# Kernel optimization log

Measured on AMD Instinct MI355X. Metric: run time of the kernel, lower is better.

The kernel has to match this reference:

```python
import jax, jax.numpy as jnp
import numpy as np

B, T, N, F, C, H, O = 4, 8, 4096, 32, 32, 64, 1
RADIUS = 50.0   # adjacency_threshold on pairwise distance
EPS = 1e-5      # batchnorm eps


def setup_inputs() -> dict:
    key = jax.random.key(0)
    ks = jax.random.split(key, 8)
    x = jax.random.normal(ks[0], (B, T, N, F), jnp.float32)
    # dist_mat from random 2D node locations in a 1000x1000 area; avg degree ~32
    loc = jax.random.uniform(ks[1], (N, 2), jnp.float32) * 1000.0
    d2 = jnp.sum((loc[:, None, :] - loc[None, :, :]) ** 2, axis=-1)  # [N,N]
    adj = (d2 < RADIUS ** 2).astype(jnp.float32)                     # includes self (d=0)
    dinv = 1.0 / jnp.sqrt(jnp.maximum(adj.sum(-1), 1.0))
    adj_norm = adj * dinv[:, None] * dinv[None, :]                   # D^-1/2 A D^-1/2
    s = 0.05
    return dict(
        x=x,
        adj_norm=adj_norm,
        bn_gamma=jnp.ones((F,), jnp.float32),
        bn_beta=jnp.zeros((F,), jnp.float32),
        W_gcn=jax.random.normal(ks[2], (F, C), jnp.float32) * s,
        b_gcn=jnp.zeros((C,), jnp.float32),
        W_ih=jax.random.normal(ks[3], (C, 3 * H), jnp.float32) * s,
        W_hh=jax.random.normal(ks[4], (H, 3 * H), jnp.float32) * s,
        b_ih=jnp.zeros((3 * H,), jnp.float32),
        b_hh=jnp.zeros((3 * H,), jnp.float32),
        W_dense=jax.random.normal(ks[5], (H, O), jnp.float32) * s,
        b_dense=jnp.zeros((O,), jnp.float32),
    )


def reference(x, adj_norm, bn_gamma, bn_beta, W_gcn, b_gcn, W_ih, W_hh, b_ih, b_hh, W_dense, b_dense):
    # BatchNorm2d over feature channel (training-mode batch stats, biased var)
    mean = x.mean(axis=(0, 1, 2))
    var = x.var(axis=(0, 1, 2))
    xn = (x - mean) * jax.lax.rsqrt(var + EPS) * bn_gamma + bn_beta  # [B,T,N,F]
    # GCN association (same math every timestep -> batch over T)
    ya = jnp.einsum('mn,btnf->btmf', adj_norm, xn)                   # neighbor aggregate
    y = jnp.einsum('btnf,fc->btnc', ya, W_gcn) + b_gcn               # [B,T,N,C]
    # precompute input-gate projections, then scan GRU cell over time
    gi = jnp.einsum('btnc,ch->btnh', y, W_ih) + b_ih                 # [B,T,N,3H]
    gi = jnp.transpose(gi, (1, 0, 2, 3))                             # [T,B,N,3H]

    def step(h, g):
        gh = h @ W_hh + b_hh
        r = jax.nn.sigmoid(g[..., :H] + gh[..., :H])
        z = jax.nn.sigmoid(g[..., H:2 * H] + gh[..., H:2 * H])
        n = jnp.tanh(g[..., 2 * H:] + r * gh[..., 2 * H:])
        h_new = (1.0 - z) * n + z * h
        return h_new, h_new

    h0 = jnp.zeros((B, N, H), x.dtype)
    _, hs = jax.lax.scan(step, h0, gi)                               # [T,B,N,H]
    out = jnp.transpose(hs, (1, 0, 2, 3)) @ W_dense + b_dense        # [B,T,N,O]
    return out
```

## Files before the change

kernel.cpp:

```cpp
#include <hip/hip_runtime.h>
#include <hip/hip_bf16.h>
#include <stdint.h>

#define B_ 4
#define T_ 8
#define N_ 4096
#define F_ 32
#define BT_ (B_*T_)
#define ROWS_ (B_*N_)
#define CAP_ 128
#define EPS_ 1e-5f
#define NELEM_ (B_*T_*N_*F_)

#define WS_BNP    0
#define WS_ROWSUM 16384
#define WS_DEG    (WS_ROWSUM + 4096)
#define WS_FRG    (WS_DEG + 4096)
#define WS_PAIR   (WS_FRG + 52*256)
#define WS_XA     (WS_PAIR + 4096*CAP_*2)
#define WS_X16    (WS_XA + NELEM_)

typedef float v4f __attribute__((ext_vector_type(4)));
typedef _Float16 half8 __attribute__((ext_vector_type(8)));
union HU { uint32_t u[4]; half8 v; };

__device__ inline float sigm_f(float x) {
  return __builtin_amdgcn_rcpf(1.0f + __expf(-x));
}
__device__ inline uint32_t f16pair(float a, float b) {
  union { _Float16 h; unsigned short s; } x, y;
  x.h = (_Float16)a; y.h = (_Float16)b;
  return (uint32_t)x.s | ((uint32_t)y.s << 16);
}
__device__ inline void sp2(float a0, float a1, uint32_t& hi, uint32_t& lo) {
  _Float16 h0 = (_Float16)a0, h1 = (_Float16)a1;
  float r0 = a0 - (float)h0, r1 = a1 - (float)h1;
  union { _Float16 h; unsigned short s; } u0, u1, v0, v1;
  u0.h = h0; u1.h = h1; v0.h = (_Float16)r0; v1.h = (_Float16)r1;
  hi = (uint32_t)u0.s | ((uint32_t)u1.s << 16);
  lo = (uint32_t)v0.s | ((uint32_t)v1.s << 16);
}

__global__ void __launch_bounds__(256)
k_pre(const float* __restrict__ x, const float* __restrict__ A, float* __restrict__ ws) {
  if (blockIdx.x < 2048) {
    int m0 = blockIdx.x * 2;
    __shared__ int cnt[2];
    __shared__ float wsum[4][2];
    if (threadIdx.x < 2) cnt[threadIdx.x] = 0;
    __syncthreads();
    int* deg = (int*)&ws[WS_DEG];
    float2* pair = (float2*)&ws[WS_PAIR];
    const float4* A4 = (const float4*)(A + (size_t)m0 * N_);
    float4 av4[8];
#pragma unroll
    for (int r = 0; r < 2; r++)
#pragma unroll
      for (int i = 0; i < 4; i++) av4[r * 4 + i] = A4[r * 1024 + threadIdx.x + 256 * i];
    float lsum[2] = {0.f, 0.f};
#pragma unroll
    for (int r = 0; r < 2; r++)
#pragma unroll
      for (int i = 0; i < 4; i++) {
        float av[4] = {av4[r*4+i].x, av4[r*4+i].y, av4[r*4+i].z, av4[r*4+i].w};
        int nb4 = (threadIdx.x + 256 * i) * 4;
#pragma unroll
        for (int e = 0; e < 4; e++) {
          float a = av[e];
          if (a != 0.0f) {
            int p = atomicAdd(&cnt[r], 1);
            if (p < CAP_) pair[(size_t)(m0 + r) * CAP_ + p] = make_float2(__int_as_float((nb4 + e) * F_), a);
            lsum[r] += a;
          }
        }
      }
#pragma unroll
    for (int r = 0; r < 2; r++) {
      float s = lsum[r];
#pragma unroll
      for (int off = 32; off > 0; off >>= 1) s += __shfl_xor(s, off, 64);
      if ((threadIdx.x & 63) == 0) wsum[threadIdx.x >> 6][r] = s;
    }
    __syncthreads();
#pragma unroll
    for (int r = 0; r < 2; r++) {
      int c = cnt[r];
      for (int p = c + threadIdx.x; p < 68; p += 256)
        pair[(size_t)(m0 + r) * CAP_ + p] = make_float2(__int_as_float(0), 0.0f);
    }
    if (threadIdx.x < 2) {
      int r = threadIdx.x;
      deg[m0 + r] = min(cnt[r], CAP_);
      ws[WS_ROWSUM + m0 + r] = wsum[0][r] + wsum[1][r] + wsum[2][r] + wsum[3][r];
    }
  } else {
    int bnb = blockIdx.x - 2048;
    const float4* x4 = (const float4*)x;
    uint2* x16 = (uint2*)(ws + WS_X16);
    int tid = bnb * 256 + threadIdx.x;
    float s[4] = {0,0,0,0}, s2[4] = {0,0,0,0};
    for (int i = tid; i < NELEM_ / 4; i += 256 * 256) {
      float4 v = x4[i];
      s[0] += v.x; s2[0] += v.x * v.x;
      s[1] += v.y; s2[1] += v.y * v.y;
      s[2] += v.z; s2[2] += v.z * v.z;
      s[3] += v.w; s2[3] += v.w * v.w;
      uint2 hp;
      hp.x = f16pair(v.x, v.y);
      hp.y = f16pair(v.z, v.w);
      x16[i] = hp;
    }
    __shared__ float ls[256][4], ls2[256][4];
#pragma unroll
    for (int r = 0; r < 4; r++) { ls[threadIdx.x][r] = s[r]; ls2[threadIdx.x][r] = s2[r]; }
    __syncthreads();
    int t = threadIdx.x;
    if (t < 32) {
      int g = t >> 2, r = t & 3;
      float a = 0.f;
      for (int q = g; q < 256; q += 8) a += ls[q][r];
      ws[WS_BNP + bnb * 64 + t] = a;
    } else if (t < 64) {
      int cch = t - 32;
      int g = cch >> 2, r = cch & 3;
      float b2 = 0.f;
      for (int q = g; q < 256; q += 8) b2 += ls2[q][r];
      ws[WS_BNP + bnb * 64 + t] = b2;
    }
  }
}

#define AGG_STEP(d) { \
    float vv = pv[d]; \
    half8 t0 = pb0[d], t1 = pb1[d]; \
    float2 p = pl[row * 69 + k + 4 + d]; \
    int off = __float_as_int(p.x) + fo; \
    pv[d] = p.y; \
    pb0[d] = *(const half8*)(xh0 + off); \
    pb1[d] = *(const half8*)(xh1 + off); \
    _Pragma("unroll") \
    for (int j = 0; j < 8; j++) { \
      acc0[j] += vv * (float)t0[j]; \
      acc1[j] += vv * (float)t1[j]; } }

__global__ void __launch_bounds__(256, 4)
k_aggf(const float* __restrict__ x, const float* __restrict__ gamma,
       const float* __restrict__ beta, const float* __restrict__ Wg,
       const float* __restrict__ bg, const float* __restrict__ Wih,
       const float* __restrict__ bih, const float* __restrict__ Whh,
       const float* __restrict__ bhh, float* __restrict__ ws) {
  __shared__ float2 pl[32 * 69];
  int tid = threadIdx.x;
  if (blockIdx.x >= 1024) {
    float* fs   = (float*)pl;
    float* bnp4 = fs;
    float* bns  = fs + 256;
    float* scl  = fs + 320;
    float* shf  = fs + 352;
    float* ps   = fs + 384;
    float* Wg_s = fs + 416;
    float* Wic  = fs + 1440;
    float* Wxc  = fs + 1952;
    float* UsV  = fs + 2464;
    float* Whc  = fs + 2496;
    int fi = blockIdx.x - 1024;
    int mt, kt;
    if (fi < 32)      { mt = fi >> 2;              kt = fi & 3; }
    else if (fi < 40) { mt = 8 + ((fi - 32) >> 1); kt = (fi & 1) ? 3 : 0; }
    else              { int r = fi - 40; mt = 12 + r / 3; kt = 1 + r % 3; }
    int cls = mt >> 2;
    int colbase = (cls < 2) ? mt * 16 : 128 + (mt & 3) * 16;
    if (kt == 1 || kt == 2) {
      for (int e = tid; e < 512; e += 256) {
        int r = e >> 4, cc = e & 15;
        Whc[e] = Whh[(size_t)((kt - 1) * 32 + r) * 192 + colbase + cc];
      }
    } else {
      ((float4*)Wg_s)[tid] = ((const float4*)Wg)[tid];
      for (int e = tid; e < 512; e += 256) {
        int r = e >> 4, cc = e & 15;
        Wic[e] = Wih[(size_t)r * 192 + colbase + cc];
      }
      int g = tid >> 6, cch = tid & 63;
      float a = 0.f;
      for (int i = 0; i < 64; i++) a += ws[WS_BNP + (size_t)(g + 4 * i) * 64 + cch];
      bnp4[g * 64 + cch] = a;
    }
    __syncthreads();
    if ((kt == 0 || kt == 3) && tid < 64)
      bns[tid] = bnp4[tid] + bnp4[64 + tid] + bnp4[128 + tid] + bnp4[192 + tid];
    __syncthreads();
    if ((kt == 0 || kt == 3) && tid < 32) {
      float cntf = (float)(B_ * T_ * N_);
      float mean = bns[tid] / cntf;
      float var = bns[32 + tid] / cntf - mean * mean;
      float sc = gamma[tid] * rsqrtf(var + EPS_);
      scl[tid] = sc;
      shf[tid] = beta[tid] - mean * sc;
    }
    __syncthreads();
    if (kt == 3 && tid < 32) {
      float acc = 0.f;
#pragma unroll
      for (int f = 0; f < 32; f++) acc += shf[f] * Wg_s[f * 32 + tid];
      ps[tid] = acc;
    }
    __syncthreads();
    if (kt == 0) {
      for (int e = tid; e < 512; e += 256) {
        int f = e >> 4, cc = e & 15;
        float acc = 0.f;
#pragma unroll
        for (int m = 0; m < 32; m++) acc += Wg_s[f * 32 + m] * Wic[m * 16 + cc];
        Wxc[e] = scl[f] * acc;
      }
    } else if (kt == 3) {
      if (tid < 16) {
        float au = 0.f;
#pragma unroll
        for (int c2 = 0; c2 < 32; c2++) au += ps[c2] * Wic[c2 * 16 + tid];
        UsV[tid] = au;
      } else if (tid < 32) {
        int cc = tid - 16;
        float av = 0.f;
#pragma unroll
        for (int c2 = 0; c2 < 32; c2++) av += bg[c2] * Wic[c2 * 16 + cc];
        UsV[16 + cc] = av + bih[colbase + cc];
      }
    }
    __syncthreads();
    if (tid < 64) {
      int L = tid, q = L >> 4, c = L & 15;
      uint32_t* wsu = (uint32_t*)ws;
#pragma unroll
      for (int d = 0; d < 4; d++) {
        float a01[2];
#pragma unroll
        for (int h2 = 0; h2 < 2; h2++) {
          int kk = q * 8 + 2 * d + h2;
          float v;
          if (kt == 0)       v = Wxc[kk * 16 + c];
          else if (kt != 3)  v = Whc[kk * 16 + c];
          else if (kk == 0)  v = (cls == 3) ? 0.f : UsV[c];
          else if (kk == 1)  v = (cls < 2) ? (UsV[16 + c] + bhh[colbase + c])
                                           : (cls == 2 ? UsV[16 + c] : bhh[colbase + c]);
          else               v = 0.f;
          a01[h2] = v;
        }
        wsu[WS_FRG + fi * 256 + L * 4 + d] = f16pair(a01[0], a01[1]);
      }
    }
    return;
  }
  int bid2 = blockIdx.x;
  int chunk = bid2 & 7;
  int mg = bid2 >> 3;
  int row = (tid >> 2) & 31;
  int f8 = tid & 3;
  int sg = tid >> 7;
  int m = mg * 32 + row;
  const int* deg = (const int*)&ws[WS_DEG];
  const float2* pair = (const float2*)&ws[WS_PAIR];
  for (int qq = tid; qq < 32 * 68; qq += 256) {
    int r = qq / 68, sl = qq - r * 68;
    pl[r * 69 + sl] = pair[(size_t)(mg * 32 + r) * CAP_ + sl];
  }
  __syncthreads();
  int d0 = deg[m];
  int dm = min(d0, 64);
  int bound = dm;
  bound = max(bound, __shfl_xor(bound, 4, 64));
  bound = max(bound, __shfl_xor(bound, 8, 64));
  bound = max(bound, __shfl_xor(bound, 16, 64));
  bound = max(bound, __shfl_xor(bound, 32, 64));
  bound = (bound + 3) & ~3;
  int bt0 = chunk * 4 + 2 * sg;
  const _Float16* xg = (const _Float16*)(ws + WS_X16);
  const _Float16* xh0 = xg + (size_t)bt0 * N_ * F_;
  const _Float16* xh1 = xh0 + N_ * F_;
  int fo = f8 * 8;
  float acc0[8], acc1[8];
#pragma unroll
  for (int j = 0; j < 8; j++) { acc0[j] = 0.f; acc1[j] = 0.f; }
  half8 pb0[4], pb1[4];
  float pv[4];
#pragma unroll
  for (int d = 0; d < 4; d++) {
    float2 p = pl[row * 69 + d];
    int off = __float_as_int(p.x) + fo;
    pv[d] = p.y;
    pb0[d] = *(const half8*)(xh0 + off);
    pb1[d] = *(const half8*)(xh1 + off);
  }
  for (int k = 0; k < bound; k += 4) {
    AGG_STEP(0) AGG_STEP(1) AGG_STEP(2) AGG_STEP(3)
  }
  if (d0 > 64) {
    for (int k = 64; k < d0; k++) {
      float2 p = pair[(size_t)m * CAP_ + k];
      int off = __float_as_int(p.x) + fo;
      float vv = p.y;
#pragma unroll
      for (int j = 0; j < 8; j++) {
        acc0[j] += vv * (float)xh0[off + j];
        acc1[j] += vv * (float)xh1[off + j];
      }
    }
  }
  size_t ob = (size_t)bt0 * N_ * F_ + m * F_ + fo;
  v4f s0a = {acc0[0], acc0[1], acc0[2], acc0[3]};
  v4f s0b = {acc0[4], acc0[5], acc0[6], acc0[7]};
  v4f s1a = {acc1[0], acc1[1], acc1[2], acc1[3]};
  v4f s1b = {acc1[4], acc1[5], acc1[6], acc1[7]};
  *(v4f*)(ws + WS_XA + ob) = s0a;
  *(v4f*)(ws + WS_XA + ob + 4) = s0b;
  *(v4f*)(ws + WS_XA + ob + (size_t)N_ * F_) = s1a;
  *(v4f*)(ws + WS_XA + ob + (size_t)N_ * F_ + 4) = s1b;
}

#define LDA(fi) (*(const half8*)(frg + (fi)*256 + L*4))
#define DO1(A_, fi, BH, BL) { half8 af = LDA(fi); \
  A_ = __builtin_amdgcn_mfma_f32_16x16x32_f16(af, BH, A_, 0, 0, 0); \
  A_ = __builtin_amdgcn_mfma_f32_16x16x32_f16(af, BL, A_, 0, 0, 0); }
#define DO1C(A_, C_, fi, BH, BL) { half8 af = LDA(fi); \
  A_ = __builtin_amdgcn_mfma_f32_16x16x32_f16(af, BH, C_, 0, 0, 0); \
  A_ = __builtin_amdgcn_mfma_f32_16x16x32_f16(af, BL, A_, 0, 0, 0); }

__global__ void __launch_bounds__(256, 2)
k_gru(const float* __restrict__ Wd, const float* __restrict__ bd,
      const float* __restrict__ ws, float* __restrict__ out) {
  __shared__ uint32_t frg[52 * 256];
  __shared__ uint32_t hx[2 * 1344];
  __shared__ float obuf[2][16];
  {
    const uint4* gf = (const uint4*)(ws + WS_FRG);
    uint4* sf = (uint4*)frg;
    for (int i = threadIdx.x; i < 52 * 64; i += 256) sf[i] = gf[i];
  }
  __syncthreads();
  int wid = threadIdx.x >> 6, L = threadIdx.x & 63;
  int grp = wid >> 1, half = wid & 1, h2 = half * 2;
  int q = L >> 4, c = L & 15;
  uint32_t* hxg = hx + grp * 1344;
  int rg0 = blockIdx.x * 32 + grp * 16;
  int b = rg0 >> 12;
  int node0 = rg0 & (N_ - 1);
  int fR0 = 4 * h2, fR1 = 4 * h2 + 4;
  int fZ0 = 16 + 4 * h2, fZ1 = 20 + 4 * h2;
  int fN0 = 32 + 2 * h2, fN1 = 34 + 2 * h2;
  int fG0 = 40 + 3 * h2, fG1 = 43 + 3 * h2;
  float wdv[2][4];
#pragma unroll
  for (int lg = 0; lg < 2; lg++)
#pragma unroll
    for (int r = 0; r < 4; r++) wdv[lg][r] = Wd[16 * (h2 + lg) + 4 * q + r];
  float bdv = bd[0];

  HU b3h, b3l;
#pragma unroll
  for (int d = 0; d < 4; d++) { b3h.u[d] = 0; b3l.u[d] = 0; }
  {
    float rsv = ws[WS_ROWSUM + node0 + c];
    uint32_t rhi, rlo;
    sp2(rsv, 1.0f, rhi, rlo);
    if (q == 0) { b3h.u[0] = rhi; b3l.u[0] = rlo & 0xFFFFu; }
  }

  v4f bias[8];
  {
    v4f z4 = {0.f, 0.f, 0.f, 0.f};
    DO1C(bias[0], z4, fR0 + 3, b3h.v, b3l.v)
    DO1C(bias[1], z4, fR1 + 3, b3h.v, b3l.v)
    DO1C(bias[2], z4, fZ0 + 3, b3h.v, b3l.v)
    DO1C(bias[3], z4, fZ1 + 3, b3h.v, b3l.v)
    DO1C(bias[4], z4, fN0 + 1, b3h.v, b3l.v)
    DO1C(bias[5], z4, fN1 + 1, b3h.v, b3l.v)
    DO1C(bias[6], z4, fG0 + 2, b3h.v, b3l.v)
    DO1C(bias[7], z4, fG1 + 2, b3h.v, b3l.v)
  }

  float h[2][4];
#pragma unroll
  for (int lg = 0; lg < 2; lg++)
#pragma unroll
    for (int r = 0; r < 4; r++) h[lg][r] = 0.f;

  const float* xab = ws + WS_XA;
  size_t xo0 = ((size_t)(b * T_) * N_ + node0 + c) * F_ + q * 8;
  float4 curA = *(const float4*)(xab + xo0);
  float4 curB = *(const float4*)(xab + xo0 + 4);
  float4 nxA, nxB;

#pragma unroll 1
  for (int t = 0; t < T_; t++) {
    HU b1h, b1l, b2h, b2l;
    if (t > 0) {
#pragma unroll
      for (int d = 0; d < 4; d++) {
        b1h.u[d] = hxg[((4 * q + d) * 2 + 0) * 21 + c];
        b1l.u[d] = hxg[((4 * q + d) * 2 + 1) * 21 + c];
        b2h.u[d] = hxg[((16 + 4 * q + d) * 2 + 0) * 21 + c];
        b2l.u[d] = hxg[((16 + 4 * q + d) * 2 + 1) * 21 + c];
      }
    }
    __syncthreads();
    if (t < T_ - 1) {
      size_t xo = ((size_t)(b * T_ + t + 1) * N_ + node0 + c) * F_ + q * 8;
      nxA = *(const float4*)(xab + xo);
      nxB = *(const float4*)(xab + xo + 4);
    }
    HU b0h, b0l;
    sp2(curA.x, curA.y, b0h.u[0], b0l.u[0]);
    sp2(curA.z, curA.w, b0h.u[1], b0l.u[1]);
    sp2(curB.x, curB.y, b0h.u[2], b0l.u[2]);
    sp2(curB.z, curB.w, b0h.u[3], b0l.u[3]);
    v4f acc[8];
    if (t > 0) {
      DO1C(acc[0], bias[0], fR0 + 1, b1h.v, b1l.v)
      DO1C(acc[1], bias[1], fR1 + 1, b1h.v, b1l.v)
      DO1C(acc[2], bias[2], fZ0 + 1, b1h.v, b1l.v)
      DO1C(acc[3], bias[3], fZ1 + 1, b1h.v, b1l.v)
      DO1C(acc[6], bias[6], fG0,     b1h.v, b1l.v)
      DO1C(acc[7], bias[7], fG1,     b1h.v, b1l.v)
      DO1(acc[0], fR0 + 2, b2h.v, b2l.v)
      DO1(acc[1], fR1 + 2, b2h.v, b2l.v)
      DO1(acc[2], fZ0 + 2, b2h.v, b2l.v)
      DO1(acc[3], fZ1 + 2, b2h.v, b2l.v)
      DO1(acc[6], fG0 + 1, b2h.v, b2l.v)
      DO1(acc[7], fG1 + 1, b2h.v, b2l.v)
      DO1(acc[0], fR0, b0h.v, b0l.v)
      DO1(acc[1], fR1, b0h.v, b0l.v)
      DO1(acc[2], fZ0, b0h.v, b0l.v)
      DO1(acc[3], fZ1, b0h.v, b0l.v)
      DO1C(acc[4], bias[4], fN0, b0h.v, b0l.v)
      DO1C(acc[5], bias[5], fN1, b0h.v, b0l.v)
    } else {
      DO1C(acc[0], bias[0], fR0, b0h.v, b0l.v)
      DO1C(acc[1], bias[1], fR1, b0h.v, b0l.v)
      DO1C(acc[2], bias[2], fZ0, b0h.v, b0l.v)
      DO1C(acc[3], bias[3], fZ1, b0h.v, b0l.v)
      DO1C(acc[4], bias[4], fN0, b0h.v, b0l.v)
      DO1C(acc[5], bias[5], fN1, b0h.v, b0l.v)
      acc[6] = bias[6]; acc[7] = bias[7];
    }
    float o = 0.f;
#pragma unroll
    for (int lg = 0; lg < 2; lg++)
#pragma unroll
      for (int r = 0; r < 4; r++) {
        float rr = sigm_f(acc[lg][r]);
        float zz = sigm_f(acc[2 + lg][r]);
        float nn = 2.0f * sigm_f(2.0f * (acc[4 + lg][r] + rr * acc[6 + lg][r])) - 1.0f;
        float hn = zz * (h[lg][r] - nn) + nn;
        h[lg][r] = hn;
        o += wdv[lg][r] * hn;
      }
    o += __shfl_xor(o, 16, 64);
    o += __shfl_xor(o, 32, 64);
    if (half == 1 && L < 16) obuf[grp][L] = o;
    if (t < T_ - 1) {
#pragma unroll
      for (int lg = 0; lg < 2; lg++)
#pragma unroll
        for (int rp = 0; rp < 2; rp++) {
          uint32_t phi, plo;
          sp2(h[lg][2 * rp], h[lg][2 * rp + 1], phi, plo);
          int pidx = 8 * (h2 + lg) + 2 * q + rp;
          hxg[(pidx * 2 + 0) * 21 + c] = phi;
          hxg[(pidx * 2 + 1) * 21 + c] = plo;
        }
    }
    __syncthreads();
    if (half == 0 && L < 16)
      out[(size_t)(b * T_ + t) * N_ + node0 + L] = o + obuf[grp][L] + bdv;
    curA = nxA; curB = nxB;
  }
}

extern "C" void kernel_launch(void* const* d_in, const int* in_sizes, int n_in,
                              void* d_out, int out_size, void* d_ws, size_t ws_size,
                              hipStream_t stream) {
  const float* x     = (const float*)d_in[0];
  const float* adj   = (const float*)d_in[1];
  const float* gamma = (const float*)d_in[2];
  const float* beta  = (const float*)d_in[3];
  const float* Wg    = (const float*)d_in[4];
  const float* bg    = (const float*)d_in[5];
  const float* Wih   = (const float*)d_in[6];
  const float* Whh   = (const float*)d_in[7];
  const float* bih   = (const float*)d_in[8];
  const float* bhh   = (const float*)d_in[9];
  const float* Wd    = (const float*)d_in[10];
  const float* bd    = (const float*)d_in[11];
  float* ws = (float*)d_ws;
  float* out = (float*)d_out;

  k_pre<<<2048 + 256, 256, 0, stream>>>(x, adj, ws);
  k_aggf<<<1024 + 52, 256, 0, stream>>>(x, gamma, beta, Wg, bg, Wih, bih, Whh, bhh, ws);
  k_gru<<<512, 256, 0, stream>>>(Wd, bd, ws, out);
}
```

Baseline: 176.8 us.

## Store fp16 features node-major across all timesteps and assign one wave per row

The fp16 copy of x is now stored node-major, with all 32 batch-time slices of a node contiguous (1 KB per node). The aggregation kernel maps each wavefront to one adjacency row, so each neighbor gather reads one contiguous 1 KB block per wave instead of scattered 64-byte pieces. Each wave iterates only its own row's degree rather than the max over 16 rows, which removes padding work. Grid size must change to N/4 blocks (1024, which matches the existing bid>=1024 split), and the transposing store in the stats kernel writes scattered 8-byte stores.

```diff
diff --git a/kernel.cpp b/kernel.cpp
--- a/kernel.cpp
+++ b/kernel.cpp
@@ -105,10 +105,11 @@
       s[1] += v.y; s2[1] += v.y * v.y;
       s[2] += v.z; s2[2] += v.z * v.z;
       s[3] += v.w; s2[3] += v.w * v.w;
+      int bt = i >> 15, rem = i & 32767, n = rem >> 3, f4 = rem & 7;
       uint2 hp;
       hp.x = f16pair(v.x, v.y);
       hp.y = f16pair(v.z, v.w);
-      x16[i] = hp;
+      x16[(size_t)(n * 32 + bt) * 8 + f4] = hp;
     }
     __shared__ float ls[256][4], ls2[256][4];
 #pragma unroll
@@ -133,11 +134,11 @@
 #define AGG_STEP(d) { \
     float vv = pv[d]; \
     half8 t0 = pb0[d], t1 = pb1[d]; \
-    float2 p = pl[row * 69 + k + 4 + d]; \
-    int off = __float_as_int(p.x) + fo; \
+    float2 p = pl[wid * 69 + k + 4 + d]; \
+    int nb = __float_as_int(p.x) << 5; \
     pv[d] = p.y; \
-    pb0[d] = *(const half8*)(xh0 + off); \
-    pb1[d] = *(const half8*)(xh1 + off); \
+    pb0[d] = *(const half8*)(xT + nb + lo0); \
+    pb1[d] = *(const half8*)(xT + nb + lo1); \
     _Pragma("unroll") \
     for (int j = 0; j < 8; j++) { \
       acc0[j] += vv * (float)t0[j]; \
@@ -252,33 +253,21 @@
     }
     return;
   }
-  int bid2 = blockIdx.x;
-  int chunk = bid2 & 7;
-  int mg = bid2 >> 3;
-  int row = (tid >> 2) & 31;
-  int f8 = tid & 3;
-  int sg = tid >> 7;
-  int m = mg * 32 + row;
+  int m0 = blockIdx.x * 4;
+  int wid = tid >> 6, L = tid & 63;
+  int m = m0 + wid;
   const int* deg = (const int*)&ws[WS_DEG];
   const float2* pair = (const float2*)&ws[WS_PAIR];
-  for (int qq = tid; qq < 32 * 68; qq += 256) {
+  for (int qq = tid; qq < 4 * 68; qq += 256) {
     int r = qq / 68, sl = qq - r * 68;
-    pl[r * 69 + sl] = pair[(size_t)(mg * 32 + r) * CAP_ + sl];
+    pl[r * 69 + sl] = pair[(size_t)(m0 + r) * CAP_ + sl];
   }
   __syncthreads();
   int d0 = deg[m];
   int dm = min(d0, 64);
-  int bound = dm;
-  bound = max(bound, __shfl_xor(bound, 4, 64));
-  bound = max(bound, __shfl_xor(bound, 8, 64));
-  bound = max(bound, __shfl_xor(bound, 16, 64));
-  bound = max(bound, __shfl_xor(bound, 32, 64));
-  bound = (bound + 3) & ~3;
-  int bt0 = chunk * 4 + 2 * sg;
-  const _Float16* xg = (const _Float16*)(ws + WS_X16);
-  const _Float16* xh0 = xg + (size_t)bt0 * N_ * F_;
-  const _Float16* xh1 = xh0 + N_ * F_;
-  int fo = f8 * 8;
+  int bound = (dm + 3) & ~3;
+  const _Float16* xT = (const _Float16*)(ws + WS_X16);
+  int lo0 = L * 8, lo1 = 512 + L * 8;
   float acc0[8], acc1[8];
 #pragma unroll
   for (int j = 0; j < 8; j++) { acc0[j] = 0.f; acc1[j] = 0.f; }
@@ -286,11 +275,11 @@
   float pv[4];
 #pragma unroll
   for (int d = 0; d < 4; d++) {
-    float2 p = pl[row * 69 + d];
-    int off = __float_as_int(p.x) + fo;
+    float2 p = pl[wid * 69 + d];
+    int nb = __float_as_int(p.x) << 5;
     pv[d] = p.y;
-    pb0[d] = *(const half8*)(xh0 + off);
-    pb1[d] = *(const half8*)(xh1 + off);
+    pb0[d] = *(const half8*)(xT + nb + lo0);
+    pb1[d] = *(const half8*)(xT + nb + lo1);
   }
   for (int k = 0; k < bound; k += 4) {
     AGG_STEP(0) AGG_STEP(1) AGG_STEP(2) AGG_STEP(3)
@@ -298,24 +287,28 @@
   if (d0 > 64) {
     for (int k = 64; k < d0; k++) {
       float2 p = pair[(size_t)m * CAP_ + k];
-      int off = __float_as_int(p.x) + fo;
+      int nb = __float_as_int(p.x) << 5;
       float vv = p.y;
+      half8 t0 = *(const half8*)(xT + nb + lo0);
+      half8 t1 = *(const half8*)(xT + nb + lo1);
 #pragma unroll
       for (int j = 0; j < 8; j++) {
-        acc0[j] += vv * (float)xh0[off + j];
-        acc1[j] += vv * (float)xh1[off + j];
-      }
-    }
-  }
-  size_t ob = (size_t)bt0 * N_ * F_ + m * F_ + fo;
-  v4f s0a = {acc0[0], acc0[1], acc0[2], acc0[3]};
-  v4f s0b = {acc0[4], acc0[5], acc0[6], acc0[7]};
-  v4f s1a = {acc1[0], acc1[1], acc1[2], acc1[3]};
-  v4f s1b = {acc1[4], acc1[5], acc1[6], acc1[7]};
-  *(v4f*)(ws + WS_XA + ob) = s0a;
-  *(v4f*)(ws + WS_XA + ob + 4) = s0b;
-  *(v4f*)(ws + WS_XA + ob + (size_t)N_ * F_) = s1a;
-  *(v4f*)(ws + WS_XA + ob + (size_t)N_ * F_ + 4) = s1b;
+        acc0[j] += vv * (float)t0[j];
+        acc1[j] += vv * (float)t1[j];
+      }
+    }
+  }
+  int s0 = L >> 2, cg = (L & 3) * 8;
+  size_t ob0 = ((size_t)s0 * N_ + m) * F_ + cg;
+  size_t ob1 = ((size_t)(s0 + 16) * N_ + m) * F_ + cg;
+  v4f w0a = {acc0[0], acc0[1], acc0[2], acc0[3]};
+  v4f w0b = {acc0[4], acc0[5], acc0[6], acc0[7]};
+  v4f w1a = {acc1[0], acc1[1], acc1[2], acc1[3]};
+  v4f w1b = {acc1[4], acc1[5], acc1[6], acc1[7]};
+  *(v4f*)(ws + WS_XA + ob0) = w0a;
+  *(v4f*)(ws + WS_XA + ob0 + 4) = w0b;
+  *(v4f*)(ws + WS_XA + ob1) = w1a;
+  *(v4f*)(ws + WS_XA + ob1 + 4) = w1b;
 }
 
 #define LDA(fi) (*(const half8*)(frg + (fi)*256 + L*4))
```

Result: faster. 167.9 us (-5.0%).
